# Kernel tuning notes

Hardware: AMD Instinct MI355X
Metric: run time of the kernel (lower is better)

Reference implementation:

```python
import jax, jax.numpy as jnp
import numpy as np

N = 120000
C = 128
NH = 4   # n_heads (hard-coded in module)
NP = 4   # n_points (hard-coded in module)
DH = C // NH
H_IMG = 192
W_IMG = 640
DFF = 512


def setup_inputs() -> dict:
    key = jax.random.key(0)
    ks = jax.random.split(key, 40)
    s = 0.02
    inp = {
        'point_features': jax.random.normal(ks[0], (N, C), jnp.float32),
        'image_feat': jax.random.normal(ks[1], (C, H_IMG, W_IMG), jnp.float32),
        'image_grid': jnp.stack([
            jax.random.randint(ks[2], (N,), 0, W_IMG, jnp.int32),
            jax.random.randint(ks[3], (N,), 0, H_IMG, jnp.int32)], axis=1),
        'pkp_w': jax.random.normal(ks[4], (C, C)) * s,
        'pkp_b': jnp.zeros((C,), jnp.float32),
        'pkp_s': jnp.ones((C,), jnp.float32),
        'pkp_t': jnp.zeros((C,), jnp.float32),
        'fc_w': jax.random.normal(ks[5], (C, 2)) * s,
        'fc_b': jnp.zeros((C,), jnp.float32),
        'fc_s': jnp.ones((C,), jnp.float32),
        'fc_t': jnp.zeros((C,), jnp.float32),
        'pt_w': jax.random.normal(ks[6], (C, C)) * s,
        'pt_b': jnp.zeros((C,), jnp.float32),
        'pt_s': jnp.ones((C,), jnp.float32),
        'pt_t': jnp.zeros((C,), jnp.float32),
        'val_w': jax.random.normal(ks[7], (C, C)) * s,
        'val_b': jnp.zeros((C,), jnp.float32),
        'off_w': jax.random.normal(ks[8], (NH * NP * 2, C)) * s,
        'off_b': jax.random.normal(ks[9], (NH * NP * 2,)) * 0.5,
        'aw_w': jax.random.normal(ks[10], (NH * NP, C)) * s,
        'aw_b': jnp.zeros((NH * NP,), jnp.float32),
        'out_w': jax.random.normal(ks[11], (C, C)) * s,
        'out_b': jnp.zeros((C,), jnp.float32),
        'ln1_g': jnp.ones((C,), jnp.float32),
        'ln1_b': jnp.zeros((C,), jnp.float32),
        'ffn_w1': jax.random.normal(ks[12], (DFF, C)) * s,
        'ffn_b1': jnp.zeros((DFF,), jnp.float32),
        'ffn_w2': jax.random.normal(ks[13], (C, DFF)) * s,
        'ffn_b2': jnp.zeros((C,), jnp.float32),
        'ln2_g': jnp.ones((C,), jnp.float32),
        'ln2_b': jnp.zeros((C,), jnp.float32),
        'fuse_w': jax.random.normal(ks[14], (C, 2 * C)) * s,
        'fuse_b': jnp.zeros((C,), jnp.float32),
        'fuse_s': jnp.ones((C,), jnp.float32),
        'fuse_t': jnp.zeros((C,), jnp.float32),
    }
    return inp


def _affine(x, s, t):
    # BatchNorm1d in eval mode folds to per-channel affine
    return x * s + t


def _ln(x, g, b):
    mu = jnp.mean(x, -1, keepdims=True)
    var = jnp.mean((x - mu) ** 2, -1, keepdims=True)
    return (x - mu) * jax.lax.rsqrt(var + 1e-5) * g + b


def _bilinear_sample(vmap, locs):
    # vmap: (H, W, NH, DH) per-head value map; locs: (N, NH, NP, 2) normalized xy
    # grid_sample semantics: align_corners=False, zero padding
    px = locs[..., 0] * W_IMG - 0.5
    py = locs[..., 1] * H_IMG - 0.5
    x0 = jnp.floor(px)
    y0 = jnp.floor(py)
    dx = px - x0
    dy = py - y0
    h_idx = jnp.arange(NH)[None, :, None]  # broadcast over (N, NH, NP)

    def gather(xi, yi):
        valid = (xi >= 0) & (xi < W_IMG) & (yi >= 0) & (yi < H_IMG)
        xc = jnp.clip(xi, 0, W_IMG - 1).astype(jnp.int32)
        yc = jnp.clip(yi, 0, H_IMG - 1).astype(jnp.int32)
        return vmap[yc, xc, h_idx] * valid[..., None]  # (N, NH, NP, DH)

    v00 = gather(x0, y0)
    v01 = gather(x0 + 1, y0)
    v10 = gather(x0, y0 + 1)
    v11 = gather(x0 + 1, y0 + 1)
    wx0 = (1 - dx)[..., None]
    wx1 = dx[..., None]
    wy0 = (1 - dy)[..., None]
    wy1 = dy[..., None]
    return (v00 * wx0 * wy0 + v01 * wx1 * wy0 + v10 * wx0 * wy1 + v11 * wx1 * wy1)


def reference(point_features, image_feat, image_grid,
              pkp_w, pkp_b, pkp_s, pkp_t,
              fc_w, fc_b, fc_s, fc_t,
              pt_w, pt_b, pt_s, pt_t,
              val_w, val_b, off_w, off_b, aw_w, aw_b, out_w, out_b,
              ln1_g, ln1_b, ffn_w1, ffn_b1, ffn_w2, ffn_b2, ln2_g, ln2_b,
              fuse_w, fuse_b, fuse_s, fuse_t):
    # 1) point feature key projection (Linear + eval-BN)
    pts = _affine(point_features @ pkp_w.T + pkp_b, pkp_s, pkp_t)

    # 2) pixel-coordinate gather of per-point image features
    gx = image_grid[:, 0]
    gy = image_grid[:, 1]
    fuse_feat = image_feat[:, gy, gx].T  # (N, C)

    # 3) normalized relative image-plane positions -> fc (Linear(2,C) + eval-BN)
    grid_f = image_grid.astype(jnp.float32)
    center = grid_f.mean(0)
    rel = grid_f - center
    mx = jnp.maximum(jnp.abs(rel).max(0), 1.0)
    pos = _affine((rel / mx) @ fc_w.T + fc_b, fc_s, fc_t)

    query = pts + pos + fuse_feat  # (N, C)

    # 4) deformable cross-attention (MSDeformAttn, 1 level, learned offsets)
    vmap = (image_feat.reshape(C, H_IMG * W_IMG).T @ val_w.T + val_b
            ).reshape(H_IMG, W_IMG, NH, DH)
    wh = jnp.array([W_IMG, H_IMG], jnp.float32)
    ref = (grid_f + 0.5) / wh  # normalized reference points (x, y)
    off = (query @ off_w.T + off_b).reshape(N, NH, NP, 2)
    locs = ref[:, None, None, :] + off / wh
    aw = jax.nn.softmax((query @ aw_w.T + aw_b).reshape(N, NH, NP), axis=-1)
    sampled = _bilinear_sample(vmap, locs)  # (N, NH, NP, DH)
    attn = (sampled * aw[..., None]).sum(2).reshape(N, C) @ out_w.T + out_b

    # transformer layer: residual + LN + FFN + LN
    q = _ln(query + attn, ln1_g, ln1_b)
    q = _ln(q + jax.nn.relu(q @ ffn_w1.T + ffn_b1) @ ffn_w2.T + ffn_b2, ln2_g, ln2_b)

    # 5) fusion_withdeform: pts_transform, concat, relu, fuse_conv
    pts_pre = _affine(point_features @ pt_w.T + pt_b, pt_s, pt_t)
    fused = jax.nn.relu(jnp.concatenate([pts_pre, q], axis=-1))  # (N, 2C)
    return jax.nn.relu(_affine(fused @ fuse_w.T + fuse_b, fuse_s, fuse_t))
```

## Files before the change

### kernel.cpp

```cpp
#include <hip/hip_runtime.h>
#include <hip/hip_bf16.h>

#define NPTS 120000
#define CC   128
#define HIMG 192
#define WIMG 640
#define HWPX (HIMG * WIMG)
#define IMIN (-2147483647 - 1)


__device__ __forceinline__ float f4get(const float4& v, int j) {
  switch (j) { case 0: return v.x; case 1: return v.y; case 2: return v.z; default: return v.w; }
}

__device__ __forceinline__ void stage_wt(float (*wt)[132], const float* __restrict__ W,
                                         int rowlen, int rowbase, int kc, int tid) {
#pragma unroll
  for (int i = 0; i < 16; ++i) {
    int idx = tid + i * 256;
    int c = idx >> 5, k = idx & 31;
    wt[k][c] = W[(size_t)(rowbase + c) * rowlen + kc + k];
  }
}

__device__ __forceinline__ void tile_fma(const float (*A)[132], int p0, int kc,
                                         const float (*wt)[132], int c0, float acc[4][4]) {
#pragma unroll
  for (int k = 0; k < 32; k += 4) {
    float4 a[4], w[4];
#pragma unroll
    for (int i = 0; i < 4; ++i) a[i] = *(const float4*)&A[p0 + i][kc + k];
#pragma unroll
    for (int kk = 0; kk < 4; ++kk) w[kk] = *(const float4*)&wt[k + kk][c0];
#pragma unroll
    for (int i = 0; i < 4; ++i) {
      float ax = a[i].x, ay = a[i].y, az = a[i].z, aw_ = a[i].w;
      acc[i][0] = fmaf(ax, w[0].x, fmaf(ay, w[1].x, fmaf(az, w[2].x, fmaf(aw_, w[3].x, acc[i][0]))));
      acc[i][1] = fmaf(ax, w[0].y, fmaf(ay, w[1].y, fmaf(az, w[2].y, fmaf(aw_, w[3].y, acc[i][1]))));
      acc[i][2] = fmaf(ax, w[0].z, fmaf(ay, w[1].z, fmaf(az, w[2].z, fmaf(aw_, w[3].z, acc[i][2]))));
      acc[i][3] = fmaf(ax, w[0].w, fmaf(ay, w[1].w, fmaf(az, w[2].w, fmaf(aw_, w[3].w, acc[i][3]))));
    }
  }
}


__global__ void k_stats_init(int* stats) {
  if (threadIdx.x == 0) {
    stats[0] = 0; stats[1] = 0;
    stats[2] = 0x7fffffff; stats[3] = IMIN;
    stats[4] = 0x7fffffff; stats[5] = IMIN;
  }
}

__global__ __launch_bounds__(256) void k_stats(const int* __restrict__ grid, int* __restrict__ stats) {
  const int2* g2 = (const int2*)grid;
  int sx = 0, sy = 0, mnx = 0x7fffffff, mxx = IMIN, mny = 0x7fffffff, mxy = IMIN;
  for (int i = blockIdx.x * 256 + threadIdx.x; i < NPTS; i += gridDim.x * 256) {
    int2 v = g2[i];
    sx += v.x; sy += v.y;
    mnx = min(mnx, v.x); mxx = max(mxx, v.x);
    mny = min(mny, v.y); mxy = max(mxy, v.y);
  }
#pragma unroll
  for (int o = 32; o >= 1; o >>= 1) {
    sx += __shfl_down(sx, o); sy += __shfl_down(sy, o);
    mnx = min(mnx, __shfl_down(mnx, o)); mxx = max(mxx, __shfl_down(mxx, o));
    mny = min(mny, __shfl_down(mny, o)); mxy = max(mxy, __shfl_down(mxy, o));
  }
  if ((threadIdx.x & 63) == 0) {
    atomicAdd(&stats[0], sx); atomicAdd(&stats[1], sy);
    atomicMin(&stats[2], mnx); atomicMax(&stats[3], mxx);
    atomicMin(&stats[4], mny); atomicMax(&stats[5], mxy);
  }
}


__global__ __launch_bounds__(256, 4) void k_vmap(
    const float* __restrict__ img, const float* __restrict__ val_w,
    const float* __restrict__ val_b, float* __restrict__ vmapT, float* __restrict__ imgT) {
  __shared__ float a_lds[32][68];
  __shared__ float wt[32][132];
  const int tid = threadIdx.x;
  const int p0 = blockIdx.x * 64;
  const int pg = tid >> 5, cg = tid & 31;
  float acc[8][4] = {};
#pragma unroll
  for (int kc = 0; kc < 128; kc += 32) {
#pragma unroll
    for (int i = 0; i < 8; ++i) {
      int idx = tid + i * 256;
      int k = idx >> 6, pp = idx & 63;
      a_lds[k][pp] = img[(size_t)(kc + k) * HWPX + p0 + pp];
    }
    stage_wt(wt, val_w, 128, 0, kc, tid);
    __syncthreads();
#pragma unroll
    for (int k = 0; k < 32; ++k) {
      float4 w = *(const float4*)&wt[k][cg * 4];
      float4 af0 = *(const float4*)&a_lds[k][pg * 8];
      float4 af1 = *(const float4*)&a_lds[k][pg * 8 + 4];
      float a8[8] = {af0.x, af0.y, af0.z, af0.w, af1.x, af1.y, af1.z, af1.w};
#pragma unroll
      for (int i = 0; i < 8; ++i) {
        acc[i][0] = fmaf(a8[i], w.x, acc[i][0]);
        acc[i][1] = fmaf(a8[i], w.y, acc[i][1]);
        acc[i][2] = fmaf(a8[i], w.z, acc[i][2]);
        acc[i][3] = fmaf(a8[i], w.w, acc[i][3]);
      }
    }
#pragma unroll
    for (int i = 0; i < 8; ++i) {
      int idx = tid + i * 256;
      int pp = idx >> 5, k = idx & 31;
      imgT[(size_t)(p0 + pp) * CC + kc + k] = a_lds[k][pp];
    }
    __syncthreads();
  }
  float4 vb = *(const float4*)&val_b[cg * 4];
  const int c = cg * 4;
  const int hh = c >> 5, d4 = c & 31;
  const int y = p0 / WIMG;
  const int xbase = p0 % WIMG + pg * 8;
#pragma unroll
  for (int i = 0; i < 8; ++i) {
    float4 o;
    o.x = acc[i][0] + vb.x; o.y = acc[i][1] + vb.y;
    o.z = acc[i][2] + vb.z; o.w = acc[i][3] + vb.w;
    *(float4*)&vmapT[(((size_t)hh * HIMG + y) * WIMG + xbase + i) * 32 + d4] = o;
  }
}


__global__ __launch_bounds__(256, 2) void k_point_a(
    const float* __restrict__ pf, const int* __restrict__ grid,
    const float* __restrict__ imgT, const float* __restrict__ vmapT,
    const int* __restrict__ stats,
    const float* __restrict__ pkp_w, const float* __restrict__ pkp_b,
    const float* __restrict__ pkp_s, const float* __restrict__ pkp_t,
    const float* __restrict__ fc_w, const float* __restrict__ fc_b,
    const float* __restrict__ fc_s, const float* __restrict__ fc_t,
    const float* __restrict__ off_w, const float* __restrict__ off_b,
    const float* __restrict__ aw_w, const float* __restrict__ aw_b,
    const float* __restrict__ out_w, const float* __restrict__ out_b,
    const float* __restrict__ ln1_g, const float* __restrict__ ln1_b,
    float* __restrict__ qout) {
  __shared__ float a_lds[32][132];
  __shared__ float q_lds[32][132];
  __shared__ float wt[32][132];
  __shared__ float off_lds[32][32];
  __shared__ float awr[32][16];
  __shared__ int gxy[64];

  const int tid = threadIdx.x;
  const int n0 = blockIdx.x * 32;
  const int pg = tid >> 5, cg = tid & 31;

#pragma unroll
  for (int i = 0; i < 4; ++i) {
    int idx = tid + i * 256;
    int p = idx >> 5, c4 = (idx & 31) << 2;
    *(float4*)&a_lds[p][c4] = *(const float4*)&pf[(size_t)(n0 + p) * CC + c4];
  }
  if (tid < 64) gxy[tid] = grid[n0 * 2 + tid];
  __syncthreads();

  float acc[4][4] = {};
#pragma unroll
  for (int kc = 0; kc < 128; kc += 32) {
    stage_wt(wt, pkp_w, 128, 0, kc, tid);
    __syncthreads();
    tile_fma(a_lds, pg * 4, kc, wt, cg * 4, acc);
    __syncthreads();
  }

  const float cx = (float)stats[0] / (float)NPTS;
  const float cy = (float)stats[1] / (float)NPTS;
  const float mxx = fmaxf(fmaxf((float)stats[3] - cx, cx - (float)stats[2]), 1.0f);
  const float mxy = fmaxf(fmaxf((float)stats[5] - cy, cy - (float)stats[4]), 1.0f);

  {
    float4 pb = *(const float4*)&pkp_b[cg * 4];
    float4 ps = *(const float4*)&pkp_s[cg * 4];
    float4 pt4 = *(const float4*)&pkp_t[cg * 4];
    float4 fbb = *(const float4*)&fc_b[cg * 4];
    float4 fss = *(const float4*)&fc_s[cg * 4];
    float4 ftt = *(const float4*)&fc_t[cg * 4];
    float4 fw0 = *(const float4*)&fc_w[cg * 8];
    float4 fw1 = *(const float4*)&fc_w[cg * 8 + 4];
    float fwx[4] = {fw0.x, fw0.z, fw1.x, fw1.z};
    float fwy[4] = {fw0.y, fw0.w, fw1.y, fw1.w};
#pragma unroll
    for (int i = 0; i < 4; ++i) {
      int p = pg * 4 + i;
      int gx = gxy[p * 2], gy = gxy[p * 2 + 1];
      float rx = ((float)gx - cx) / mxx;
      float ry = ((float)gy - cy) / mxy;
      float4 ff = *(const float4*)&imgT[(size_t)(gy * WIMG + gx) * CC + cg * 4];
#pragma unroll
      for (int j = 0; j < 4; ++j) {
        float qv = (acc[i][j] + f4get(pb, j)) * f4get(ps, j) + f4get(pt4, j);
        float pos = (rx * fwx[j] + ry * fwy[j] + f4get(fbb, j)) * f4get(fss, j) + f4get(ftt, j);
        q_lds[p][cg * 4 + j] = qv + pos + f4get(ff, j);
      }
    }
  }
  __syncthreads();

  {
    int p = tid >> 3, g = tid & 7;
    float accO[4] = {}; float accA[2] = {};
    const float* qrow = q_lds[p];
#pragma unroll 8
    for (int k = 0; k < 128; k += 4) {
      float4 qv = *(const float4*)&qrow[k];
#pragma unroll
      for (int r = 0; r < 4; ++r) {
        float4 w = *(const float4*)&off_w[(size_t)(g * 4 + r) * 128 + k];
        accO[r] = fmaf(qv.x, w.x, fmaf(qv.y, w.y, fmaf(qv.z, w.z, fmaf(qv.w, w.w, accO[r]))));
      }
#pragma unroll
      for (int r = 0; r < 2; ++r) {
        float4 w = *(const float4*)&aw_w[(size_t)(g * 2 + r) * 128 + k];
        accA[r] = fmaf(qv.x, w.x, fmaf(qv.y, w.y, fmaf(qv.z, w.z, fmaf(qv.w, w.w, accA[r]))));
      }
    }
#pragma unroll
    for (int r = 0; r < 4; ++r) off_lds[p][g * 4 + r] = accO[r] + off_b[g * 4 + r];
#pragma unroll
    for (int r = 0; r < 2; ++r) awr[p][g * 2 + r] = accA[r] + aw_b[g * 2 + r];
  }
  __syncthreads();

  {
    int pr = tid >> 1, half = tid & 1;
    int p = pr >> 2, h = pr & 3;
    float w0 = awr[p][h * 4 + 0], w1 = awr[p][h * 4 + 1];
    float w2 = awr[p][h * 4 + 2], w3 = awr[p][h * 4 + 3];
    float m = fmaxf(fmaxf(w0, w1), fmaxf(w2, w3));
    float e0 = expf(w0 - m), e1 = expf(w1 - m), e2 = expf(w2 - m), e3 = expf(w3 - m);
    float inv = 1.0f / (e0 + e1 + e2 + e3);
    float awn[4] = {e0 * inv, e1 * inv, e2 * inv, e3 * inv};
    float gxf = (float)gxy[p * 2], gyf = (float)gxy[p * 2 + 1];
    float accd[16] = {};
    const float* vbase = vmapT + (size_t)h * HIMG * WIMG * 32 + half * 16;
#pragma unroll
    for (int np = 0; np < 4; ++np) {
      float ox = off_lds[p][(h * 4 + np) * 2 + 0];
      float oy = off_lds[p][(h * 4 + np) * 2 + 1];
      float lx = (gxf + 0.5f) * (1.0f / WIMG) + ox * (1.0f / WIMG);
      float ly = (gyf + 0.5f) * (1.0f / HIMG) + oy * (1.0f / HIMG);
      float px = lx * (float)WIMG - 0.5f;
      float py = ly * (float)HIMG - 0.5f;
      float x0f = floorf(px), y0f = floorf(py);
      float dx = px - x0f, dy = py - y0f;
      float x1f = x0f + 1.0f, y1f = y0f + 1.0f;
      bool vx0 = (x0f >= 0.f) && (x0f < (float)WIMG);
      bool vx1 = (x1f >= 0.f) && (x1f < (float)WIMG);
      bool vy0 = (y0f >= 0.f) && (y0f < (float)HIMG);
      bool vy1 = (y1f >= 0.f) && (y1f < (float)HIMG);
      int x0c = (int)fminf(fmaxf(x0f, 0.f), (float)(WIMG - 1));
      int x1c = (int)fminf(fmaxf(x1f, 0.f), (float)(WIMG - 1));
      int y0c = (int)fminf(fmaxf(y0f, 0.f), (float)(HIMG - 1));
      int y1c = (int)fminf(fmaxf(y1f, 0.f), (float)(HIMG - 1));
      float a = awn[np];
      float c00 = (vx0 && vy0) ? a * (1.f - dx) * (1.f - dy) : 0.f;
      float c01 = (vx1 && vy0) ? a * dx * (1.f - dy) : 0.f;
      float c10 = (vx0 && vy1) ? a * (1.f - dx) * dy : 0.f;
      float c11 = (vx1 && vy1) ? a * dx * dy : 0.f;
      const float* p00 = vbase + ((size_t)y0c * WIMG + x0c) * 32;
      const float* p01 = vbase + ((size_t)y0c * WIMG + x1c) * 32;
      const float* p10 = vbase + ((size_t)y1c * WIMG + x0c) * 32;
      const float* p11 = vbase + ((size_t)y1c * WIMG + x1c) * 32;
#pragma unroll
      for (int q4 = 0; q4 < 4; ++q4) {
        float4 v00 = *(const float4*)&p00[q4 * 4];
        float4 v01 = *(const float4*)&p01[q4 * 4];
        float4 v10 = *(const float4*)&p10[q4 * 4];
        float4 v11 = *(const float4*)&p11[q4 * 4];
        accd[q4 * 4 + 0] = fmaf(c00, v00.x, fmaf(c01, v01.x, fmaf(c10, v10.x, fmaf(c11, v11.x, accd[q4 * 4 + 0]))));
        accd[q4 * 4 + 1] = fmaf(c00, v00.y, fmaf(c01, v01.y, fmaf(c10, v10.y, fmaf(c11, v11.y, accd[q4 * 4 + 1]))));
        accd[q4 * 4 + 2] = fmaf(c00, v00.z, fmaf(c01, v01.z, fmaf(c10, v10.z, fmaf(c11, v11.z, accd[q4 * 4 + 2]))));
        accd[q4 * 4 + 3] = fmaf(c00, v00.w, fmaf(c01, v01.w, fmaf(c10, v10.w, fmaf(c11, v11.w, accd[q4 * 4 + 3]))));
      }
    }
#pragma unroll
    for (int q4 = 0; q4 < 4; ++q4) {
      *(float4*)&a_lds[p][h * 32 + half * 16 + q4 * 4] =
          make_float4(accd[q4 * 4 + 0], accd[q4 * 4 + 1], accd[q4 * 4 + 2], accd[q4 * 4 + 3]);
    }
  }
  __syncthreads();

  float acc2[4][4] = {};
#pragma unroll
  for (int kc = 0; kc < 128; kc += 32) {
    stage_wt(wt, out_w, 128, 0, kc, tid);
    __syncthreads();
    tile_fma(a_lds, pg * 4, kc, wt, cg * 4, acc2);
    __syncthreads();
  }
  {
    float4 ob = *(const float4*)&out_b[cg * 4];
#pragma unroll
    for (int i = 0; i < 4; ++i) {
      int p = pg * 4 + i;
#pragma unroll
      for (int j = 0; j < 4; ++j)
        q_lds[p][cg * 4 + j] += acc2[i][j] + f4get(ob, j);
    }
  }
  __syncthreads();

  {
    int p = tid >> 3, l = tid & 7, c0 = l * 16;
    float v[16];
#pragma unroll
    for (int q4 = 0; q4 < 4; ++q4) {
      float4 t = *(const float4*)&q_lds[p][c0 + q4 * 4];
      v[q4 * 4 + 0] = t.x; v[q4 * 4 + 1] = t.y; v[q4 * 4 + 2] = t.z; v[q4 * 4 + 3] = t.w;
    }
    float s = 0.f, ss = 0.f;
#pragma unroll
    for (int i = 0; i < 16; ++i) { s += v[i]; ss += v[i] * v[i]; }
#pragma unroll
    for (int mm = 1; mm <= 4; mm <<= 1) { s += __shfl_xor(s, mm); ss += __shfl_xor(ss, mm); }
    float mu = s * (1.0f / 128.0f);
    float var = ss * (1.0f / 128.0f) - mu * mu;
    float rstd = rsqrtf(var + 1e-5f);
#pragma unroll
    for (int q4 = 0; q4 < 4; ++q4) {
      int c = c0 + q4 * 4;
      float4 g = *(const float4*)&ln1_g[c];
      float4 b = *(const float4*)&ln1_b[c];
      float4 o;
      o.x = (v[q4 * 4 + 0] - mu) * rstd * g.x + b.x;
      o.y = (v[q4 * 4 + 1] - mu) * rstd * g.y + b.y;
      o.z = (v[q4 * 4 + 2] - mu) * rstd * g.z + b.z;
      o.w = (v[q4 * 4 + 3] - mu) * rstd * g.w + b.w;
      *(float4*)&qout[(size_t)(n0 + p) * CC + c] = o;
    }
  }
}


__global__ __launch_bounds__(256, 3) void k_ffn(
    float* __restrict__ qio, const float* __restrict__ w1, const float* __restrict__ b1,
    const float* __restrict__ w2, const float* __restrict__ b2,
    const float* __restrict__ g2, const float* __restrict__ bb2) {
  __shared__ float q_lds[32][132];
  __shared__ float h_lds[32][132];
  __shared__ float wt[32][132];
  const int tid = threadIdx.x;
  const int n0 = blockIdx.x * 32;
  const int pg = tid >> 5, cg = tid & 31;
#pragma unroll
  for (int i = 0; i < 4; ++i) {
    int idx = tid + i * 256;
    int p = idx >> 5, c4 = (idx & 31) << 2;
    *(float4*)&q_lds[p][c4] = *(const float4*)&qio[(size_t)(n0 + p) * CC + c4];
  }
  __syncthreads();
  float acc[4][4] = {};
#pragma unroll
  for (int jc = 0; jc < 4; ++jc) {
    float acc2[4][4] = {};
#pragma unroll
    for (int kc = 0; kc < 128; kc += 32) {
      stage_wt(wt, w1, 128, jc * 128, kc, tid);
      __syncthreads();
      tile_fma(q_lds, pg * 4, kc, wt, cg * 4, acc2);
      __syncthreads();
    }
    float4 bb = *(const float4*)&b1[jc * 128 + cg * 4];
#pragma unroll
    for (int i = 0; i < 4; ++i)
#pragma unroll
      for (int j = 0; j < 4; ++j)
        h_lds[pg * 4 + i][cg * 4 + j] = fmaxf(acc2[i][j] + f4get(bb, j), 0.f);
    __syncthreads();
#pragma unroll
    for (int kc = 0; kc < 128; kc += 32) {
      stage_wt(wt, w2, 512, 0, jc * 128 + kc, tid);
      __syncthreads();
      tile_fma(h_lds, pg * 4, kc, wt, cg * 4, acc);
      __syncthreads();
    }
  }
  {
    float4 b2v = *(const float4*)&b2[cg * 4];
#pragma unroll
    for (int i = 0; i < 4; ++i)
#pragma unroll
      for (int j = 0; j < 4; ++j)
        h_lds[pg * 4 + i][cg * 4 + j] = q_lds[pg * 4 + i][cg * 4 + j] + acc[i][j] + f4get(b2v, j);
  }
  __syncthreads();
  {
    int p = tid >> 3, l = tid & 7, c0 = l * 16;
    float v[16];
#pragma unroll
    for (int q4 = 0; q4 < 4; ++q4) {
      float4 t = *(const float4*)&h_lds[p][c0 + q4 * 4];
      v[q4 * 4 + 0] = t.x; v[q4 * 4 + 1] = t.y; v[q4 * 4 + 2] = t.z; v[q4 * 4 + 3] = t.w;
    }
    float s = 0.f, ss = 0.f;
#pragma unroll
    for (int i = 0; i < 16; ++i) { s += v[i]; ss += v[i] * v[i]; }
#pragma unroll
    for (int mm = 1; mm <= 4; mm <<= 1) { s += __shfl_xor(s, mm); ss += __shfl_xor(ss, mm); }
    float mu = s * (1.0f / 128.0f);
    float var = ss * (1.0f / 128.0f) - mu * mu;
    float rstd = rsqrtf(var + 1e-5f);
#pragma unroll
    for (int q4 = 0; q4 < 4; ++q4) {
      int c = c0 + q4 * 4;
      float4 g = *(const float4*)&g2[c];
      float4 b = *(const float4*)&bb2[c];
      float4 o;
      o.x = (v[q4 * 4 + 0] - mu) * rstd * g.x + b.x;
      o.y = (v[q4 * 4 + 1] - mu) * rstd * g.y + b.y;
      o.z = (v[q4 * 4 + 2] - mu) * rstd * g.z + b.z;
      o.w = (v[q4 * 4 + 3] - mu) * rstd * g.w + b.w;
      *(float4*)&qio[(size_t)(n0 + p) * CC + c] = o;
    }
  }
}


__global__ __launch_bounds__(256, 3) void k_final(
    const float* __restrict__ pf, const float* __restrict__ q,
    const float* __restrict__ pt_w, const float* __restrict__ pt_b,
    const float* __restrict__ pt_s, const float* __restrict__ pt_t,
    const float* __restrict__ fuse_w, const float* __restrict__ fuse_b,
    const float* __restrict__ fuse_s, const float* __restrict__ fuse_t,
    float* __restrict__ outp) {
  __shared__ float a_lds[32][132];
  __shared__ float q_lds[32][132];
  __shared__ float wt[32][132];
  const int tid = threadIdx.x;
  const int n0 = blockIdx.x * 32;
  const int pg = tid >> 5, cg = tid & 31;
#pragma unroll
  for (int i = 0; i < 4; ++i) {
    int idx = tid + i * 256;
    int p = idx >> 5, c4 = (idx & 31) << 2;
    *(float4*)&a_lds[p][c4] = *(const float4*)&pf[(size_t)(n0 + p) * CC + c4];
    float4 qq = *(const float4*)&q[(size_t)(n0 + p) * CC + c4];
    qq.x = fmaxf(qq.x, 0.f); qq.y = fmaxf(qq.y, 0.f);
    qq.z = fmaxf(qq.z, 0.f); qq.w = fmaxf(qq.w, 0.f);
    *(float4*)&q_lds[p][c4] = qq;
  }
  __syncthreads();
  float accP[4][4] = {};
#pragma unroll
  for (int kc = 0; kc < 128; kc += 32) {
    stage_wt(wt, pt_w, 128, 0, kc, tid);
    __syncthreads();
    tile_fma(a_lds, pg * 4, kc, wt, cg * 4, accP);
    __syncthreads();
  }
  {
    float4 pb = *(const float4*)&pt_b[cg * 4];
    float4 ps = *(const float4*)&pt_s[cg * 4];
    float4 pt4 = *(const float4*)&pt_t[cg * 4];
#pragma unroll
    for (int i = 0; i < 4; ++i)
#pragma unroll
      for (int j = 0; j < 4; ++j)
        a_lds[pg * 4 + i][cg * 4 + j] =
            fmaxf((accP[i][j] + f4get(pb, j)) * f4get(ps, j) + f4get(pt4, j), 0.f);
  }
  __syncthreads();
  float acc[4][4] = {};
#pragma unroll
  for (int kc = 0; kc < 128; kc += 32) {
    stage_wt(wt, fuse_w, 256, 0, kc, tid);
    __syncthreads();
    tile_fma(a_lds, pg * 4, kc, wt, cg * 4, acc);
    __syncthreads();
  }
#pragma unroll
  for (int kc = 0; kc < 128; kc += 32) {
    stage_wt(wt, fuse_w, 256, 0, 128 + kc, tid);
    __syncthreads();
    tile_fma(q_lds, pg * 4, kc, wt, cg * 4, acc);
    __syncthreads();
  }
  {
    float4 fb = *(const float4*)&fuse_b[cg * 4];
    float4 fs = *(const float4*)&fuse_s[cg * 4];
    float4 ft = *(const float4*)&fuse_t[cg * 4];
#pragma unroll
    for (int i = 0; i < 4; ++i) {
      float4 o;
      o.x = fmaxf((acc[i][0] + fb.x) * fs.x + ft.x, 0.f);
      o.y = fmaxf((acc[i][1] + fb.y) * fs.y + ft.y, 0.f);
      o.z = fmaxf((acc[i][2] + fb.z) * fs.z + ft.z, 0.f);
      o.w = fmaxf((acc[i][3] + fb.w) * fs.w + ft.w, 0.f);
      *(float4*)&outp[(size_t)(n0 + pg * 4 + i) * CC + cg * 4] = o;
    }
  }
}


extern "C" void kernel_launch(void* const* d_in, const int* in_sizes, int n_in,
                              void* d_out, int out_size, void* d_ws, size_t ws_size,
                              hipStream_t stream) {
  const float* pf    = (const float*)d_in[0];
  const float* img   = (const float*)d_in[1];
  const int*   grid  = (const int*)d_in[2];
  const float* pkp_w = (const float*)d_in[3];
  const float* pkp_b = (const float*)d_in[4];
  const float* pkp_s = (const float*)d_in[5];
  const float* pkp_t = (const float*)d_in[6];
  const float* fc_w  = (const float*)d_in[7];
  const float* fc_b  = (const float*)d_in[8];
  const float* fc_s  = (const float*)d_in[9];
  const float* fc_t  = (const float*)d_in[10];
  const float* pt_w  = (const float*)d_in[11];
  const float* pt_b  = (const float*)d_in[12];
  const float* pt_s  = (const float*)d_in[13];
  const float* pt_t  = (const float*)d_in[14];
  const float* val_w = (const float*)d_in[15];
  const float* val_b = (const float*)d_in[16];
  const float* off_w = (const float*)d_in[17];
  const float* off_b = (const float*)d_in[18];
  const float* aw_w  = (const float*)d_in[19];
  const float* aw_b  = (const float*)d_in[20];
  const float* out_w = (const float*)d_in[21];
  const float* out_b = (const float*)d_in[22];
  const float* ln1_g = (const float*)d_in[23];
  const float* ln1_b = (const float*)d_in[24];
  const float* ffn_w1 = (const float*)d_in[25];
  const float* ffn_b1 = (const float*)d_in[26];
  const float* ffn_w2 = (const float*)d_in[27];
  const float* ffn_b2 = (const float*)d_in[28];
  const float* ln2_g = (const float*)d_in[29];
  const float* ln2_b = (const float*)d_in[30];
  const float* fuse_w = (const float*)d_in[31];
  const float* fuse_b = (const float*)d_in[32];
  const float* fuse_s = (const float*)d_in[33];
  const float* fuse_t = (const float*)d_in[34];
  float* outp = (float*)d_out;

  char* ws = (char*)d_ws;
  int* stats   = (int*)ws;
  float* vmapT = (float*)(ws + 256);
  float* imgT  = vmapT + (size_t)4 * HIMG * WIMG * 32;
  float* qbuf  = imgT + (size_t)HWPX * CC;

  k_stats_init<<<1, 64, 0, stream>>>(stats);
  k_stats<<<256, 256, 0, stream>>>(grid, stats);
  k_vmap<<<HWPX / 64, 256, 0, stream>>>(img, val_w, val_b, vmapT, imgT);
  k_point_a<<<NPTS / 32, 256, 0, stream>>>(pf, grid, imgT, vmapT, stats,
                                           pkp_w, pkp_b, pkp_s, pkp_t,
                                           fc_w, fc_b, fc_s, fc_t,
                                           off_w, off_b, aw_w, aw_b,
                                           out_w, out_b, ln1_g, ln1_b, qbuf);
  k_ffn<<<NPTS / 32, 256, 0, stream>>>(qbuf, ffn_w1, ffn_b1, ffn_w2, ffn_b2, ln2_g, ln2_b);
  k_final<<<NPTS / 32, 256, 0, stream>>>(pf, qbuf, pt_w, pt_b, pt_s, pt_t,
                                         fuse_w, fuse_b, fuse_s, fuse_t, outp);
}
```

Baseline: 2.020 ms.

## Store value map in fp16 and split sampling into a standalone kernel

The projected value map is now written as half precision, halving its footprint and the bytes gathered during bilinear sampling. The point kernel is split in two: a query kernel writes query, pixel-space sample positions and softmaxed attention weights to global buffers, and a separate lightweight k_sample kernel does the gather with more threads per launch. The out-projection and LN1 are merged into the FFN kernel. This trades extra global round trips (query, positions, weights, sampled features) and fp16 rounding of value features for better gather occupancy and less gather bandwidth.

```diff
diff --git a/kernel.cpp b/kernel.cpp
--- a/kernel.cpp
+++ b/kernel.cpp
@@ -1,5 +1,6 @@
 #include <hip/hip_runtime.h>
 #include <hip/hip_bf16.h>
+#include <hip/hip_fp16.h>
 
 #define NPTS 120000
 #define CC   128
@@ -77,7 +78,7 @@
 
 __global__ __launch_bounds__(256, 4) void k_vmap(
     const float* __restrict__ img, const float* __restrict__ val_w,
-    const float* __restrict__ val_b, float* __restrict__ vmapT, float* __restrict__ imgT) {
+    const float* __restrict__ val_b, __half* __restrict__ vmapT, float* __restrict__ imgT) {
   __shared__ float a_lds[32][68];
   __shared__ float wt[32][132];
   const int tid = threadIdx.x;
@@ -123,31 +124,27 @@
   const int xbase = p0 % WIMG + pg * 8;
 #pragma unroll
   for (int i = 0; i < 8; ++i) {
-    float4 o;
-    o.x = acc[i][0] + vb.x; o.y = acc[i][1] + vb.y;
-    o.z = acc[i][2] + vb.z; o.w = acc[i][3] + vb.w;
-    *(float4*)&vmapT[(((size_t)hh * HIMG + y) * WIMG + xbase + i) * 32 + d4] = o;
-  }
-}
-
-
-__global__ __launch_bounds__(256, 2) void k_point_a(
+    union { __half2 h2[2]; float2 f2; } pk;
+    pk.h2[0] = __floats2half2_rn(acc[i][0] + vb.x, acc[i][1] + vb.y);
+    pk.h2[1] = __floats2half2_rn(acc[i][2] + vb.z, acc[i][3] + vb.w);
+    *(float2*)&vmapT[(((size_t)hh * HIMG + y) * WIMG + xbase + i) * 32 + d4] = pk.f2;
+  }
+}
+
+
+__global__ __launch_bounds__(256, 3) void k_query(
     const float* __restrict__ pf, const int* __restrict__ grid,
-    const float* __restrict__ imgT, const float* __restrict__ vmapT,
-    const int* __restrict__ stats,
+    const float* __restrict__ imgT, const int* __restrict__ stats,
     const float* __restrict__ pkp_w, const float* __restrict__ pkp_b,
     const float* __restrict__ pkp_s, const float* __restrict__ pkp_t,
     const float* __restrict__ fc_w, const float* __restrict__ fc_b,
     const float* __restrict__ fc_s, const float* __restrict__ fc_t,
     const float* __restrict__ off_w, const float* __restrict__ off_b,
     const float* __restrict__ aw_w, const float* __restrict__ aw_b,
-    const float* __restrict__ out_w, const float* __restrict__ out_b,
-    const float* __restrict__ ln1_g, const float* __restrict__ ln1_b,
-    float* __restrict__ qout) {
+    float* __restrict__ qout, float* __restrict__ pxyb, float* __restrict__ awb) {
   __shared__ float a_lds[32][132];
   __shared__ float q_lds[32][132];
   __shared__ float wt[32][132];
-  __shared__ float off_lds[32][32];
   __shared__ float awr[32][16];
   __shared__ int gxy[64];
 
@@ -224,70 +221,118 @@
         accA[r] = fmaf(qv.x, w.x, fmaf(qv.y, w.y, fmaf(qv.z, w.z, fmaf(qv.w, w.w, accA[r]))));
       }
     }
-#pragma unroll
-    for (int r = 0; r < 4; ++r) off_lds[p][g * 4 + r] = accO[r] + off_b[g * 4 + r];
+    float gxf = (float)gxy[p * 2], gyf = (float)gxy[p * 2 + 1];
+    float4 o;
+    o.x = accO[0] + off_b[g * 4 + 0] + gxf;
+    o.y = accO[1] + off_b[g * 4 + 1] + gyf;
+    o.z = accO[2] + off_b[g * 4 + 2] + gxf;
+    o.w = accO[3] + off_b[g * 4 + 3] + gyf;
+    *(float4*)&pxyb[(size_t)(n0 + p) * 32 + g * 4] = o;
 #pragma unroll
     for (int r = 0; r < 2; ++r) awr[p][g * 2 + r] = accA[r] + aw_b[g * 2 + r];
   }
   __syncthreads();
 
-  {
-    int pr = tid >> 1, half = tid & 1;
-    int p = pr >> 2, h = pr & 3;
+  if (tid < 128) {
+    int p = tid >> 2, h = tid & 3;
     float w0 = awr[p][h * 4 + 0], w1 = awr[p][h * 4 + 1];
     float w2 = awr[p][h * 4 + 2], w3 = awr[p][h * 4 + 3];
     float m = fmaxf(fmaxf(w0, w1), fmaxf(w2, w3));
     float e0 = expf(w0 - m), e1 = expf(w1 - m), e2 = expf(w2 - m), e3 = expf(w3 - m);
     float inv = 1.0f / (e0 + e1 + e2 + e3);
-    float awn[4] = {e0 * inv, e1 * inv, e2 * inv, e3 * inv};
-    float gxf = (float)gxy[p * 2], gyf = (float)gxy[p * 2 + 1];
-    float accd[16] = {};
-    const float* vbase = vmapT + (size_t)h * HIMG * WIMG * 32 + half * 16;
-#pragma unroll
-    for (int np = 0; np < 4; ++np) {
-      float ox = off_lds[p][(h * 4 + np) * 2 + 0];
-      float oy = off_lds[p][(h * 4 + np) * 2 + 1];
-      float lx = (gxf + 0.5f) * (1.0f / WIMG) + ox * (1.0f / WIMG);
-      float ly = (gyf + 0.5f) * (1.0f / HIMG) + oy * (1.0f / HIMG);
-      float px = lx * (float)WIMG - 0.5f;
-      float py = ly * (float)HIMG - 0.5f;
-      float x0f = floorf(px), y0f = floorf(py);
-      float dx = px - x0f, dy = py - y0f;
-      float x1f = x0f + 1.0f, y1f = y0f + 1.0f;
-      bool vx0 = (x0f >= 0.f) && (x0f < (float)WIMG);
-      bool vx1 = (x1f >= 0.f) && (x1f < (float)WIMG);
-      bool vy0 = (y0f >= 0.f) && (y0f < (float)HIMG);
-      bool vy1 = (y1f >= 0.f) && (y1f < (float)HIMG);
-      int x0c = (int)fminf(fmaxf(x0f, 0.f), (float)(WIMG - 1));
-      int x1c = (int)fminf(fmaxf(x1f, 0.f), (float)(WIMG - 1));
-      int y0c = (int)fminf(fmaxf(y0f, 0.f), (float)(HIMG - 1));
-      int y1c = (int)fminf(fmaxf(y1f, 0.f), (float)(HIMG - 1));
-      float a = awn[np];
-      float c00 = (vx0 && vy0) ? a * (1.f - dx) * (1.f - dy) : 0.f;
-      float c01 = (vx1 && vy0) ? a * dx * (1.f - dy) : 0.f;
-      float c10 = (vx0 && vy1) ? a * (1.f - dx) * dy : 0.f;
-      float c11 = (vx1 && vy1) ? a * dx * dy : 0.f;
-      const float* p00 = vbase + ((size_t)y0c * WIMG + x0c) * 32;
-      const float* p01 = vbase + ((size_t)y0c * WIMG + x1c) * 32;
-      const float* p10 = vbase + ((size_t)y1c * WIMG + x0c) * 32;
-      const float* p11 = vbase + ((size_t)y1c * WIMG + x1c) * 32;
-#pragma unroll
-      for (int q4 = 0; q4 < 4; ++q4) {
-        float4 v00 = *(const float4*)&p00[q4 * 4];
-        float4 v01 = *(const float4*)&p01[q4 * 4];
-        float4 v10 = *(const float4*)&p10[q4 * 4];
-        float4 v11 = *(const float4*)&p11[q4 * 4];
-        accd[q4 * 4 + 0] = fmaf(c00, v00.x, fmaf(c01, v01.x, fmaf(c10, v10.x, fmaf(c11, v11.x, accd[q4 * 4 + 0]))));
-        accd[q4 * 4 + 1] = fmaf(c00, v00.y, fmaf(c01, v01.y, fmaf(c10, v10.y, fmaf(c11, v11.y, accd[q4 * 4 + 1]))));
-        accd[q4 * 4 + 2] = fmaf(c00, v00.z, fmaf(c01, v01.z, fmaf(c10, v10.z, fmaf(c11, v11.z, accd[q4 * 4 + 2]))));
-        accd[q4 * 4 + 3] = fmaf(c00, v00.w, fmaf(c01, v01.w, fmaf(c10, v10.w, fmaf(c11, v11.w, accd[q4 * 4 + 3]))));
+    *(float4*)&awb[(size_t)(n0 + p) * 16 + h * 4] =
+        make_float4(e0 * inv, e1 * inv, e2 * inv, e3 * inv);
+  }
+
+#pragma unroll
+  for (int i = 0; i < 4; ++i) {
+    int idx = tid + i * 256;
+    int p = idx >> 5, c4 = (idx & 31) << 2;
+    *(float4*)&qout[(size_t)(n0 + p) * CC + c4] = *(const float4*)&q_lds[p][c4];
+  }
+}
+
+
+__global__ __launch_bounds__(256, 5) void k_sample(
+    const float* __restrict__ pxyb, const float* __restrict__ awb,
+    const __half* __restrict__ vmapT, float* __restrict__ sbuf) {
+  const int gid = blockIdx.x * 256 + threadIdx.x;
+  const int half = gid & 1, h = (gid >> 1) & 3, p = gid >> 3;
+  const float4* pxr = (const float4*)(pxyb + (size_t)p * 32 + h * 8);
+  float4 pa = pxr[0], pb = pxr[1];
+  float4 awv = *(const float4*)(awb + (size_t)p * 16 + h * 4);
+  float pxs[4] = {pa.x, pa.z, pb.x, pb.z};
+  float pys[4] = {pa.y, pa.w, pb.y, pb.w};
+  float aws[4] = {awv.x, awv.y, awv.z, awv.w};
+  float accd[16] = {};
+  const __half* vbase = vmapT + (size_t)h * HWPX * 32 + half * 16;
+#pragma unroll
+  for (int np = 0; np < 4; ++np) {
+    float px = pxs[np], py = pys[np];
+    float x0f = floorf(px), y0f = floorf(py);
+    float dx = px - x0f, dy = py - y0f;
+    float x1f = x0f + 1.0f, y1f = y0f + 1.0f;
+    bool vx0 = (x0f >= 0.f) && (x0f < (float)WIMG);
+    bool vx1 = (x1f >= 0.f) && (x1f < (float)WIMG);
+    bool vy0 = (y0f >= 0.f) && (y0f < (float)HIMG);
+    bool vy1 = (y1f >= 0.f) && (y1f < (float)HIMG);
+    int x0c = (int)fminf(fmaxf(x0f, 0.f), (float)(WIMG - 1));
+    int x1c = (int)fminf(fmaxf(x1f, 0.f), (float)(WIMG - 1));
+    int y0c = (int)fminf(fmaxf(y0f, 0.f), (float)(HIMG - 1));
+    int y1c = (int)fminf(fmaxf(y1f, 0.f), (float)(HIMG - 1));
+    float a = aws[np];
+    float c00 = (vx0 && vy0) ? a * (1.f - dx) * (1.f - dy) : 0.f;
+    float c01 = (vx1 && vy0) ? a * dx * (1.f - dy) : 0.f;
+    float c10 = (vx0 && vy1) ? a * (1.f - dx) * dy : 0.f;
+    float c11 = (vx1 && vy1) ? a * dx * dy : 0.f;
+    const float4* t00 = (const float4*)(vbase + (size_t)(y0c * WIMG + x0c) * 32);
+    const float4* t01 = (const float4*)(vbase + (size_t)(y0c * WIMG + x1c) * 32);
+    const float4* t10 = (const float4*)(vbase + (size_t)(y1c * WIMG + x0c) * 32);
+    const float4* t11 = (const float4*)(vbase + (size_t)(y1c * WIMG + x1c) * 32);
+#pragma unroll
+    for (int qq = 0; qq < 2; ++qq) {
+      union U { float4 f; __half2 h2[4]; };
+      U u00, u01, u10, u11;
+      u00.f = t00[qq]; u01.f = t01[qq]; u10.f = t10[qq]; u11.f = t11[qq];
+#pragma unroll
+      for (int j = 0; j < 4; ++j) {
+        float2 w00 = __half22float2(u00.h2[j]);
+        float2 w01 = __half22float2(u01.h2[j]);
+        float2 w10 = __half22float2(u10.h2[j]);
+        float2 w11 = __half22float2(u11.h2[j]);
+        int c = qq * 8 + j * 2;
+        accd[c]     = fmaf(c00, w00.x, fmaf(c01, w01.x, fmaf(c10, w10.x, fmaf(c11, w11.x, accd[c]))));
+        accd[c + 1] = fmaf(c00, w00.y, fmaf(c01, w01.y, fmaf(c10, w10.y, fmaf(c11, w11.y, accd[c + 1]))));
       }
     }
-#pragma unroll
-    for (int q4 = 0; q4 < 4; ++q4) {
-      *(float4*)&a_lds[p][h * 32 + half * 16 + q4 * 4] =
-          make_float4(accd[q4 * 4 + 0], accd[q4 * 4 + 1], accd[q4 * 4 + 2], accd[q4 * 4 + 3]);
-    }
+  }
+  float* out = sbuf + (size_t)p * CC + h * 32 + half * 16;
+#pragma unroll
+  for (int q4 = 0; q4 < 4; ++q4)
+    *(float4*)(out + q4 * 4) =
+        make_float4(accd[q4 * 4 + 0], accd[q4 * 4 + 1], accd[q4 * 4 + 2], accd[q4 * 4 + 3]);
+}
+
+
+__global__ __launch_bounds__(256, 3) void k_ffn2(
+    const float* __restrict__ sbuf, float* __restrict__ qio,
+    const float* __restrict__ out_w, const float* __restrict__ out_b,
+    const float* __restrict__ ln1_g, const float* __restrict__ ln1_b,
+    const float* __restrict__ w1, const float* __restrict__ b1,
+    const float* __restrict__ w2, const float* __restrict__ b2,
+    const float* __restrict__ g2, const float* __restrict__ bb2) {
+  __shared__ float a_lds[32][132];
+  __shared__ float q_lds[32][132];
+  __shared__ float wt[32][132];
+  const int tid = threadIdx.x;
+  const int n0 = blockIdx.x * 32;
+  const int pg = tid >> 5, cg = tid & 31;
+#pragma unroll
+  for (int i = 0; i < 4; ++i) {
+    int idx = tid + i * 256;
+    int p = idx >> 5, c4 = (idx & 31) << 2;
+    *(float4*)&a_lds[p][c4] = *(const float4*)&sbuf[(size_t)(n0 + p) * CC + c4];
+    *(float4*)&q_lds[p][c4] = *(const float4*)&qio[(size_t)(n0 + p) * CC + c4];
   }
   __syncthreads();
 
@@ -302,12 +347,10 @@
   {
     float4 ob = *(const float4*)&out_b[cg * 4];
 #pragma unroll
-    for (int i = 0; i < 4; ++i) {
-      int p = pg * 4 + i;
+    for (int i = 0; i < 4; ++i)
 #pragma unroll
       for (int j = 0; j < 4; ++j)
-        q_lds[p][cg * 4 + j] += acc2[i][j] + f4get(ob, j);
-    }
+        q_lds[pg * 4 + i][cg * 4 + j] += acc2[i][j] + f4get(ob, j);
   }
   __syncthreads();
 
@@ -337,38 +380,20 @@
       o.y = (v[q4 * 4 + 1] - mu) * rstd * g.y + b.y;
       o.z = (v[q4 * 4 + 2] - mu) * rstd * g.z + b.z;
       o.w = (v[q4 * 4 + 3] - mu) * rstd * g.w + b.w;
-      *(float4*)&qout[(size_t)(n0 + p) * CC + c] = o;
-    }
-  }
-}
-
-
-__global__ __launch_bounds__(256, 3) void k_ffn(
-    float* __restrict__ qio, const float* __restrict__ w1, const float* __restrict__ b1,
-    const float* __restrict__ w2, const float* __restrict__ b2,
-    const float* __restrict__ g2, const float* __restrict__ bb2) {
-  __shared__ float q_lds[32][132];
-  __shared__ float h_lds[32][132];
-  __shared__ float wt[32][132];
-  const int tid = threadIdx.x;
-  const int n0 = blockIdx.x * 32;
-  const int pg = tid >> 5, cg = tid & 31;
-#pragma unroll
-  for (int i = 0; i < 4; ++i) {
-    int idx = tid + i * 256;
-    int p = idx >> 5, c4 = (idx & 31) << 2;
-    *(float4*)&q_lds[p][c4] = *(const float4*)&qio[(size_t)(n0 + p) * CC + c4];
-  }
-  __syncthreads();
+      *(float4*)&q_lds[p][c] = o;
+    }
+  }
+  __syncthreads();
+
   float acc[4][4] = {};
 #pragma unroll
   for (int jc = 0; jc < 4; ++jc) {
-    float acc2[4][4] = {};
+    float acch[4][4] = {};
 #pragma unroll
     for (int kc = 0; kc < 128; kc += 32) {
       stage_wt(wt, w1, 128, jc * 128, kc, tid);
       __syncthreads();
-      tile_fma(q_lds, pg * 4, kc, wt, cg * 4, acc2);
+      tile_fma(q_lds, pg * 4, kc, wt, cg * 4, acch);
       __syncthreads();
     }
     float4 bb = *(const float4*)&b1[jc * 128 + cg * 4];
@@ -376,13 +401,13 @@
     for (int i = 0; i < 4; ++i)
 #pragma unroll
       for (int j = 0; j < 4; ++j)
-        h_lds[pg * 4 + i][cg * 4 + j] = fmaxf(acc2[i][j] + f4get(bb, j), 0.f);
+        a_lds[pg * 4 + i][cg * 4 + j] = fmaxf(acch[i][j] + f4get(bb, j), 0.f);
     __syncthreads();
 #pragma unroll
     for (int kc = 0; kc < 128; kc += 32) {
       stage_wt(wt, w2, 512, 0, jc * 128 + kc, tid);
       __syncthreads();
-      tile_fma(h_lds, pg * 4, kc, wt, cg * 4, acc);
+      tile_fma(a_lds, pg * 4, kc, wt, cg * 4, acc);
       __syncthreads();
     }
   }
@@ -392,7 +417,8 @@
     for (int i = 0; i < 4; ++i)
 #pragma unroll
       for (int j = 0; j < 4; ++j)
-        h_lds[pg * 4 + i][cg * 4 + j] = q_lds[pg * 4 + i][cg * 4 + j] + acc[i][j] + f4get(b2v, j);
+        a_lds[pg * 4 + i][cg * 4 + j] =
+            q_lds[pg * 4 + i][cg * 4 + j] + acc[i][j] + f4get(b2v, j);
   }
   __syncthreads();
   {
@@ -400,7 +426,7 @@
     float v[16];
 #pragma unroll
     for (int q4 = 0; q4 < 4; ++q4) {
-      float4 t = *(const float4*)&h_lds[p][c0 + q4 * 4];
+      float4 t = *(const float4*)&a_lds[p][c0 + q4 * 4];
       v[q4 * 4 + 0] = t.x; v[q4 * 4 + 1] = t.y; v[q4 * 4 + 2] = t.z; v[q4 * 4 + 3] = t.w;
     }
     float s = 0.f, ss = 0.f;
@@ -544,20 +570,25 @@
   float* outp = (float*)d_out;
 
   char* ws = (char*)d_ws;
-  int* stats   = (int*)ws;
-  float* vmapT = (float*)(ws + 256);
-  float* imgT  = vmapT + (size_t)4 * HIMG * WIMG * 32;
-  float* qbuf  = imgT + (size_t)HWPX * CC;
+  int* stats    = (int*)ws;
+  __half* vmapT = (__half*)(ws + 256);
+  float* imgT   = (float*)(ws + 256 + (size_t)4 * HWPX * 32 * sizeof(__half));
+  float* sbuf   = imgT;
+  float* qbuf   = imgT + (size_t)HWPX * CC;
+  float* pxyb   = qbuf + (size_t)NPTS * CC;
+  float* awb    = pxyb + (size_t)NPTS * 32;
 
   k_stats_init<<<1, 64, 0, stream>>>(stats);
   k_stats<<<256, 256, 0, stream>>>(grid, stats);
   k_vmap<<<HWPX / 64, 256, 0, stream>>>(img, val_w, val_b, vmapT, imgT);
-  k_point_a<<<NPTS / 32, 256, 0, stream>>>(pf, grid, imgT, vmapT, stats,
-                                           pkp_w, pkp_b, pkp_s, pkp_t,
-                                           fc_w, fc_b, fc_s, fc_t,
-                                           off_w, off_b, aw_w, aw_b,
-                                           out_w, out_b, ln1_g, ln1_b, qbuf);
-  k_ffn<<<NPTS / 32, 256, 0, stream>>>(qbuf, ffn_w1, ffn_b1, ffn_w2, ffn_b2, ln2_g, ln2_b);
+  k_query<<<NPTS / 32, 256, 0, stream>>>(pf, grid, imgT, stats,
+                                         pkp_w, pkp_b, pkp_s, pkp_t,
+                                         fc_w, fc_b, fc_s, fc_t,
+                                         off_w, off_b, aw_w, aw_b,
+                                         qbuf, pxyb, awb);
+  k_sample<<<(NPTS * 8) / 256, 256, 0, stream>>>(pxyb, awb, vmapT, sbuf);
+  k_ffn2<<<NPTS / 32, 256, 0, stream>>>(sbuf, qbuf, out_w, out_b, ln1_g, ln1_b,
+                                        ffn_w1, ffn_b1, ffn_w2, ffn_b2, ln2_g, ln2_b);
   k_final<<<NPTS / 32, 256, 0, stream>>>(pf, qbuf, pt_w, pt_b, pt_s, pt_t,
                                          fuse_w, fuse_b, fuse_s, fuse_t, outp);
 }
```

New measurement: 1.835 ms. 9.2% less time.
